# Kernel tuning notes

Hardware: AMD Instinct MI355X
Metric: run time of the kernel (lower is better)

The kernel has to match this reference:

```python
import jax, jax.numpy as jnp
import numpy as np

B, L, D_IN, D_MODEL, D_STATE, D_DISCR, KER = 2, 1024, 512, 1024, 16, 64, 4


def setup_inputs() -> dict:
    ks = jax.random.split(jax.random.key(0), 9)
    s = 0.02
    return {
        "seq": jax.random.normal(ks[0], (B, L, D_IN), jnp.float32),
        "W_in": jax.random.normal(ks[1], (2 * D_MODEL, D_IN), jnp.float32) * s,
        "W_out": jax.random.normal(ks[2], (D_IN, D_MODEL), jnp.float32) * s,
        "W_B": jax.random.normal(ks[3], (D_STATE, D_MODEL), jnp.float32) * s,
        "W_C": jax.random.normal(ks[4], (D_STATE, D_MODEL), jnp.float32) * s,
        "W_D1": jax.random.normal(ks[5], (D_DISCR, D_MODEL), jnp.float32) * s,
        "W_D2": jax.random.normal(ks[6], (D_MODEL, D_DISCR), jnp.float32) * s,
        "conv_w": jax.random.normal(ks[7], (D_MODEL, 1, KER), jnp.float32) * 0.1,
        "conv_b": jax.random.normal(ks[8], (D_MODEL,), jnp.float32) * 0.01,
        "A": jnp.tile(jnp.arange(1, D_STATE + 1, dtype=jnp.float32), (D_MODEL, 1)),
        "D": jnp.ones((D_MODEL,), jnp.float32),
    }


def _causal_depthwise_conv(x, w, b):
    # x: [B, L, D] -> torch Conv1d(groups=D, padding=KER-1) truncated to first L outputs
    x = jnp.swapaxes(x, 1, 2)  # [B, D, L]
    y = jax.lax.conv_general_dilated(
        x, w, window_strides=(1,), padding=[(KER - 1, 0)],
        dimension_numbers=("NCH", "OIH", "NCH"), feature_group_count=D_MODEL)
    y = y + b[None, :, None]
    return jnp.swapaxes(y, 1, 2)  # [B, L, D]


def _ssm(x, W_B, W_C, W_D1, W_D2, A, D):
    # x: [B, L, D]
    exp_negA = jnp.exp(-A)                                  # [D, S]
    Bm = jnp.einsum("bld,sd->bls", x, W_B)                  # [B, L, S]
    Cm = jnp.einsum("bld,sd->bls", x, W_C)                  # [B, L, S]
    delta = jax.nn.softplus(D + jnp.einsum("ble,de->bld", jnp.einsum("bld,ed->ble", x, W_D1), W_D2))  # [B, L, D]
    A_bar = exp_negA[None, None] * delta[..., None]         # [B, L, D, S]
    X = Bm[:, :, None, :] * delta[..., None] * x[..., None]  # [B, L, D, S]

    def comb(c1, c2):
        a1, x1 = c1
        a2, x2 = c2
        return a1 * a2, a2 * x1 + x2

    _, h = jax.lax.associative_scan(comb, (A_bar, X), axis=1)  # h: [B, L, D, S]
    y = jnp.einsum("blds,bls->bld", h, Cm)
    return y + D * x


def reference(seq, W_in, W_out, W_B, W_C, W_D1, W_D2, conv_w, conv_b, A, D):
    ab = jnp.einsum("bli,oi->blo", seq, W_in)   # [B, L, 2*D_MODEL]
    a, b = ab[..., :D_MODEL], ab[..., D_MODEL:]
    a = jax.nn.silu(_causal_depthwise_conv(a, conv_w, conv_b))
    a = _ssm(a, W_B, W_C, W_D1, W_D2, A, D)
    out = a * jax.nn.silu(b)
    return jnp.einsum("bld,od->blo", out, W_out)  # [B, L, D_IN]
```

## Files before the change

### kernel.cpp

```cpp
#include <hip/hip_runtime.h>
#include <hip/hip_bf16.h>

typedef short short8 __attribute__((ext_vector_type(8)));
typedef short short4v __attribute__((ext_vector_type(4)));
typedef float float4v __attribute__((ext_vector_type(4)));

#define B_   2
#define L_   1024
#define DIN  512
#define DM   1024
#define DS   16
#define DD   64
#define KER_ 4
#define NROW (B_*L_)

#define SD   4
#define SC   128
#define SLC  8
#define NSEG 8

__device__ __forceinline__ float silu_f(float v){ return v / (1.f + expf(-v)); }

__device__ __forceinline__ short2 f2bf2(float a, float b) {
  __hip_bfloat162 h = __float22bfloat162_rn(float2{a, b});
  union { __hip_bfloat162 h; short2 s; } u; u.h = h; return u.s;
}
__device__ __forceinline__ short f2bf1(float a) {
  __hip_bfloat16 h = __float2bfloat16(a);
  union { __hip_bfloat16 h; short s; } u; u.h = h; return u.s;
}
__device__ __forceinline__ short8 pack8(const float4& x0, const float4& x1) {
  short2 s0 = f2bf2(x0.x, x0.y), s1 = f2bf2(x0.z, x0.w);
  short2 s2 = f2bf2(x1.x, x1.y), s3 = f2bf2(x1.z, x1.w);
  return short8{ s0.x, s0.y, s1.x, s1.y, s2.x, s2.y, s3.x, s3.y };
}
__device__ __forceinline__ float bf2f(short s) {
  union { unsigned u; float f; } v; v.u = ((unsigned)(unsigned short)s) << 16; return v.f;
}

__global__ __launch_bounds__(512)
void gemm1_k(const float* __restrict__ seq, const float* __restrict__ Win,
             __hip_bfloat16* __restrict__ ab, float* __restrict__ pall) {
  __shared__ short As[128 * 40];
  __shared__ short Bs[128 * 40];
  const int tid  = threadIdx.x;
  {
    int zi = (blockIdx.y * 16 + blockIdx.x) * 1024 + tid * 2;
    if (zi < NROW * 96) { pall[zi] = 0.f; pall[zi + 1] = 0.f; }
  }
  const int lane = tid & 63;
  const int wave = tid >> 6;
  const int r16  = lane & 15;
  const int quad = lane >> 4;
  const int m0 = blockIdx.y * 128;
  const int n0 = blockIdx.x * 128;
  const int wm = wave & 1;
  const int wn = wave >> 1;
  float4v acc[4][2];
#pragma unroll
  for (int i = 0; i < 4; i++)
#pragma unroll
    for (int j = 0; j < 2; j++) acc[i][j] = (float4v){0.f, 0.f, 0.f, 0.f};
  const int row = tid >> 2, q = tid & 3;
  float4 pfA0, pfA1, pfB0, pfB1;
  auto ldu = [&](int k0) {
    const float4* pa = (const float4*)(seq + (size_t)(m0 + row) * DIN + k0 + q * 8);
    pfA0 = pa[0]; pfA1 = pa[1];
    const float4* pb = (const float4*)(Win + (size_t)(n0 + row) * DIN + k0 + q * 8);
    pfB0 = pb[0]; pfB1 = pb[1];
  };
  auto stu = [&]() {
    *(short8*)&As[row * 40 + q * 8] = pack8(pfA0, pfA1);
    *(short8*)&Bs[row * 40 + q * 8] = pack8(pfB0, pfB1);
  };
  ldu(0);
  for (int k0 = 0; k0 < DIN; k0 += 32) {
    stu();
    __syncthreads();
    if (k0 + 32 < DIN) ldu(k0 + 32);
    short8 afr[4], bfr[2];
#pragma unroll
    for (int mi = 0; mi < 4; mi++)
      afr[mi] = *(const short8*)&As[(wm * 64 + mi * 16 + r16) * 40 + quad * 8];
#pragma unroll
    for (int ni = 0; ni < 2; ni++)
      bfr[ni] = *(const short8*)&Bs[(wn * 32 + ni * 16 + r16) * 40 + quad * 8];
#pragma unroll
    for (int mi = 0; mi < 4; mi++)
#pragma unroll
      for (int ni = 0; ni < 2; ni++)
        acc[mi][ni] = __builtin_amdgcn_mfma_f32_16x16x32_bf16(afr[mi], bfr[ni], acc[mi][ni], 0, 0, 0);
    __syncthreads();
  }
#pragma unroll
  for (int mi = 0; mi < 4; mi++)
#pragma unroll
    for (int ni = 0; ni < 2; ni++) {
      int gn = n0 + wn * 32 + ni * 16 + r16;
#pragma unroll
      for (int r = 0; r < 4; r++) {
        int gm = m0 + wm * 64 + mi * 16 + quad * 4 + r;
        ab[(size_t)gm * (2 * DM) + gn] = __float2bfloat16(acc[mi][ni][r]);
      }
    }
}

__global__ __launch_bounds__(256)
void convproj_k(const __hip_bfloat16* __restrict__ ab, const float* __restrict__ cw,
                const float* __restrict__ cb, const float* __restrict__ WB,
                const float* __restrict__ WC, const float* __restrict__ WD1,
                float* __restrict__ xt, short* __restrict__ gt,
                float* __restrict__ pall) {
  __shared__ char smraw[12800];
  const int blk = blockIdx.x;
  const int tid = threadIdx.x;

  if (blk < 1024) {
    short* tile = (short*)smraw;
    const int n0 = (blk & 31) * 64;
    const int d0 = (blk >> 5) * 64;
    const int l0 = n0 & (L_ - 1);
    for (int u = tid; u < 67 * 8; u += 256) {
      int r = u >> 3, c8 = u & 7;
      int l = l0 - 3 + r;
      short8 v = short8{0, 0, 0, 0, 0, 0, 0, 0};
      if (l >= 0 && r < 67)
        v = *(const short8*)(ab + (size_t)(n0 - l0 + l) * (2 * DM) + d0 + c8 * 8);
      *(short8*)&tile[r * 72 + c8 * 8] = v;
    }
    __syncthreads();
    const int i  = tid & 63;
    const int dl = tid >> 6;
    if (d0 < DM) {
#pragma unroll
      for (int p8 = 0; p8 < 2; p8++) {
        const int dc0 = dl * 16 + p8 * 8;
        short8 t0 = *(const short8*)&tile[(i + 0) * 72 + dc0];
        short8 t1 = *(const short8*)&tile[(i + 1) * 72 + dc0];
        short8 t2 = *(const short8*)&tile[(i + 2) * 72 + dc0];
        short8 t3 = *(const short8*)&tile[(i + 3) * 72 + dc0];
#pragma unroll
        for (int e = 0; e < 8; e++) {
          int d = d0 + dc0 + e;
          float4 w = *(const float4*)(cw + d * 4);
          float a = cb[d];
          a += bf2f(t0[e]) * w.x;
          a += bf2f(t1[e]) * w.y;
          a += bf2f(t2[e]) * w.z;
          a += bf2f(t3[e]) * w.w;
          xt[(size_t)d * NROW + n0 + i] = silu_f(a);
        }
      }
    } else {
#pragma unroll
      for (int p8 = 0; p8 < 2; p8++) {
        const int dc0 = dl * 16 + p8 * 8;
        short8 v = *(const short8*)&tile[(i + 3) * 72 + dc0];
#pragma unroll
        for (int e = 0; e < 8; e++)
          gt[(size_t)(d0 - DM + dc0 + e) * NROW + n0 + i] = v[e];
      }
    }
    return;
  }

  short* As = (short*)smraw;
  short* Bs = As + 64 * 40;
  const int b2   = blk - 1024;
  const int lane = tid & 63;
  const int wave = tid >> 6;
  const int r16  = lane & 15;
  const int quad = lane >> 4;
  const int m0   = (b2 & 31) * 64;
  const int kbeg = (b2 >> 5) * 128;
  float4v acc[6];
#pragma unroll
  for (int i = 0; i < 6; i++) acc[i] = (float4v){0.f, 0.f, 0.f, 0.f};

  short8 ta[KER_];
  float4 pf0[2], pf1[2];
  const int arow = tid >> 2, aq = tid & 3;
  const int an = m0 + arow, al = an & (L_ - 1), abq = an >> 10;

  auto ldu_a = [&](int k0) {
#pragma unroll
    for (int t = 0; t < KER_; t++) {
      int ll = al - (KER_ - 1) + t;
      if (ll >= 0)
        ta[t] = *(const short8*)(ab + (size_t)(abq * L_ + ll) * (2 * DM) + k0 + aq * 8);
      else
        ta[t] = short8{0, 0, 0, 0, 0, 0, 0, 0};
    }
  };
  auto stu_a = [&](int k0) {
    float r8[8];
#pragma unroll
    for (int e = 0; e < 8; e++) {
      int d = k0 + aq * 8 + e;
      float4 w = *(const float4*)(cw + d * 4);
      float a = cb[d];
      a += bf2f(ta[0][e]) * w.x;
      a += bf2f(ta[1][e]) * w.y;
      a += bf2f(ta[2][e]) * w.z;
      a += bf2f(ta[3][e]) * w.w;
      r8[e] = silu_f(a);
    }
    *(short8*)&As[arow * 40 + aq * 8] =
        pack8(float4{r8[0], r8[1], r8[2], r8[3]}, float4{r8[4], r8[5], r8[6], r8[7]});
  };
  auto ldu_b = [&](int j, int k0) {
    int u = tid + j * 256;
    if (u >= 640) return;
    int v = u - 256, row = v >> 2, q = v & 3;
    const float* bp = (row < 16) ? (WB + (size_t)row * DM)
                    : (row < 32) ? (WC + (size_t)(row - 16) * DM)
                                 : (WD1 + (size_t)(row - 32) * DM);
    const float4* p = (const float4*)(bp + k0 + q * 8);
    pf0[j - 1] = p[0]; pf1[j - 1] = p[1];
  };
  auto stu_b = [&](int j) {
    int u = tid + j * 256;
    if (u >= 640) return;
    int v = u - 256, row = v >> 2, q = v & 3;
    *(short8*)&Bs[row * 40 + q * 8] = pack8(pf0[j - 1], pf1[j - 1]);
  };

  ldu_a(kbeg); ldu_b(1, kbeg); ldu_b(2, kbeg);
  for (int k0 = kbeg; k0 < kbeg + 128; k0 += 32) {
    stu_a(k0); stu_b(1); stu_b(2);
    __syncthreads();
    if (k0 + 32 < kbeg + 128) { ldu_a(k0 + 32); ldu_b(1, k0 + 32); ldu_b(2, k0 + 32); }
    short8 afr = *(const short8*)&As[(wave * 16 + r16) * 40 + quad * 8];
#pragma unroll
    for (int ni = 0; ni < 6; ni++) {
      short8 bfr = *(const short8*)&Bs[(ni * 16 + r16) * 40 + quad * 8];
      acc[ni] = __builtin_amdgcn_mfma_f32_16x16x32_bf16(afr, bfr, acc[ni], 0, 0, 0);
    }
    __syncthreads();
  }
#pragma unroll
  for (int ni = 0; ni < 6; ni++) {
    int gn = ni * 16 + r16;
#pragma unroll
    for (int r = 0; r < 4; r++) {
      int gm = m0 + wave * 16 + quad * 4 + r;
      atomicAdd(&pall[(size_t)gm * 96 + gn], acc[ni][r]);
    }
  }
}

__global__ __launch_bounds__(256)
void delta_k(const float* __restrict__ t1, const float* __restrict__ WD2,
             const float* __restrict__ Dv, float* __restrict__ dltT) {
  __shared__ short As[64 * 40];
  __shared__ short Bs[64 * 40];
  const int tid  = threadIdx.x;
  const int lane = tid & 63;
  const int wave = tid >> 6;
  const int r16  = lane & 15;
  const int quad = lane >> 4;
  const int m0 = blockIdx.y * 64;
  const int n0 = blockIdx.x * 64;
  const int wm = wave & 1, wn = wave >> 1;
  float4v acc[2][2];
#pragma unroll
  for (int i = 0; i < 2; i++)
#pragma unroll
    for (int j = 0; j < 2; j++) acc[i][j] = (float4v){0.f, 0.f, 0.f, 0.f};
  float4 pf0[2], pf1[2];
  auto ldu = [&](int j, int k0) {
    int u = tid + j * 256;
    const float4* p;
    if (u < 256) { int row = u >> 2, q = u & 3;
      p = (const float4*)(t1 + (size_t)(m0 + row) * 96 + k0 + q * 8);
    } else { int v = u - 256; int row = v >> 2, q = v & 3;
      p = (const float4*)(WD2 + (size_t)(n0 + row) * DD + k0 + q * 8);
    }
    pf0[j] = p[0]; pf1[j] = p[1];
  };
  auto stu = [&](int j) {
    int u = tid + j * 256;
    short8 s = pack8(pf0[j], pf1[j]);
    if (u < 256) { int row = u >> 2, q = u & 3; *(short8*)&As[row * 40 + q * 8] = s; }
    else { int v = u - 256; int row = v >> 2, q = v & 3; *(short8*)&Bs[row * 40 + q * 8] = s; }
  };
  ldu(0, 0); ldu(1, 0);
  for (int k0 = 0; k0 < DD; k0 += 32) {
    stu(0); stu(1);
    __syncthreads();
    if (k0 + 32 < DD) { ldu(0, k0 + 32); ldu(1, k0 + 32); }
    short8 afr[2], bfr[2];
#pragma unroll
    for (int mi = 0; mi < 2; mi++)
      afr[mi] = *(const short8*)&As[(wm * 32 + mi * 16 + r16) * 40 + quad * 8];
#pragma unroll
    for (int ni = 0; ni < 2; ni++)
      bfr[ni] = *(const short8*)&Bs[(wn * 32 + ni * 16 + r16) * 40 + quad * 8];
#pragma unroll
    for (int mi = 0; mi < 2; mi++)
#pragma unroll
      for (int ni = 0; ni < 2; ni++)
        acc[mi][ni] = __builtin_amdgcn_mfma_f32_16x16x32_bf16(afr[mi], bfr[ni], acc[mi][ni], 0, 0, 0);
    __syncthreads();
  }
#pragma unroll
  for (int mi = 0; mi < 2; mi++)
#pragma unroll
    for (int ni = 0; ni < 2; ni++) {
      int gn = n0 + wn * 32 + ni * 16 + r16;
      float dvn = Dv[gn];
#pragma unroll
      for (int r = 0; r < 4; r++) {
        int gm = m0 + wm * 32 + mi * 16 + quad * 4 + r;
        float v = acc[mi][ni][r] + dvn;
        v = fmaxf(v, 0.f) + log1pf(expf(-fabsf(v)));
        dltT[(size_t)gn * NROW + gm] = v;
      }
    }
}

__global__ __launch_bounds__(512, 2)
void scan_fused_k(const float* __restrict__ xt, const float* __restrict__ dltT,
                  const float* __restrict__ pall, const float* __restrict__ A,
                  const float* __restrict__ Dv, const short* __restrict__ gt,
                  short* __restrict__ soutb) {
  __shared__ float Pl[DS * SD][SC + 1];
  __shared__ float Hl[DS * SD][SC + 1];
  __shared__ float Ps[DS * SD][NSEG + 1];
  __shared__ float Hs[DS * SD][NSEG + 1];
  const int blk = blockIdx.x;
  const int b   = blk >> 8;
  const int d0  = (blk & 255) * SD;
  const int dd  = threadIdx.x & (SD - 1);
  const int c   = threadIdx.x >> 2;
  const int d   = d0 + dd;

  float e[DS];
#pragma unroll
  for (int s = 0; s < DS; s++) e[s] = expf(-A[d * DS + s]);

  const int nbase = b * L_ + c * SLC;
  const float* xrow = xt   + (size_t)d * NROW;
  const float* drow = dltT + (size_t)d * NROW;
  const short* grow = gt   + (size_t)d * NROW;

  float h[DS];
#pragma unroll
  for (int s = 0; s < DS; s++) h[s] = 0.f;
  float pdl = 1.f;
#pragma unroll
  for (int q = 0; q < SLC / 4; q++) {
    const int n = nbase + q * 4;
    float4 x4 = *(const float4*)(xrow + n);
    float4 d4 = *(const float4*)(drow + n);
    float4 bq[4][4];
#pragma unroll
    for (int t = 0; t < 4; t++) {
      const float4* pp = (const float4*)(pall + (size_t)(n + t) * 96);
      bq[t][0] = pp[0]; bq[t][1] = pp[1]; bq[t][2] = pp[2]; bq[t][3] = pp[3];
    }
#pragma unroll
    for (int t = 0; t < 4; t++) {
      float dl = (&d4.x)[t], xv = (&x4.x)[t];
      float dx = dl * xv;
      pdl *= dl;
      float bmv[DS] = { bq[t][0].x, bq[t][0].y, bq[t][0].z, bq[t][0].w,
                        bq[t][1].x, bq[t][1].y, bq[t][1].z, bq[t][1].w,
                        bq[t][2].x, bq[t][2].y, bq[t][2].z, bq[t][2].w,
                        bq[t][3].x, bq[t][3].y, bq[t][3].z, bq[t][3].w };
#pragma unroll
      for (int s = 0; s < DS; s++)
        h[s] = (e[s] * dl) * h[s] + bmv[s] * dx;
    }
  }
#pragma unroll
  for (int s = 0; s < DS; s++) {
    float e2 = e[s] * e[s], e4 = e2 * e2, e8 = e4 * e4;
    Pl[dd * DS + s][c] = e8 * pdl;
    Hl[dd * DS + s][c] = h[s];
  }
  __syncthreads();

  {
    const int seg = threadIdx.x >> 6;
    const int cmb = threadIdx.x & 63;
    float* Prow = &Pl[cmb][0];
    float* Hrow = &Hl[cmb][0];
    float Pa = 1.f, Ha = 0.f;
#pragma unroll
    for (int i = 0; i < SC / NSEG; i++) {
      int c2 = seg * (SC / NSEG) + i;
      float p = Prow[c2], hh = Hrow[c2];
      Prow[c2] = Pa;
      Hrow[c2] = Ha;
      Ha = p * Ha + hh;
      Pa *= p;
    }
    Ps[cmb][seg] = Pa;
    Hs[cmb][seg] = Ha;
  }
  __syncthreads();

  if (threadIdx.x < DS * SD) {
    float* Pr = &Ps[threadIdx.x][0];
    float* Hr = &Hs[threadIdx.x][0];
    float H = 0.f;
#pragma unroll
    for (int g = 0; g < NSEG; g++) {
      float p = Pr[g], hh = Hr[g];
      Hr[g] = H;
      H = p * H + hh;
    }
  }
  __syncthreads();

  const float Dd = Dv[d];
  {
    const int g = c >> 4;
#pragma unroll
    for (int s = 0; s < DS; s++)
      h[s] = Pl[dd * DS + s][c] * Hs[dd * DS + s][g] + Hl[dd * DS + s][c];
  }
#pragma unroll
  for (int q = 0; q < SLC / 4; q++) {
    const int n = nbase + q * 4;
    float4 x4 = *(const float4*)(xrow + n);
    float4 d4 = *(const float4*)(drow + n);
    short4v g4 = *(const short4v*)(grow + n);
    float4 bq[4][4], cq[4][4];
#pragma unroll
    for (int t = 0; t < 4; t++) {
      const float4* pp = (const float4*)(pall + (size_t)(n + t) * 96);
      bq[t][0] = pp[0]; bq[t][1] = pp[1]; bq[t][2] = pp[2]; bq[t][3] = pp[3];
      cq[t][0] = pp[4]; cq[t][1] = pp[5]; cq[t][2] = pp[6]; cq[t][3] = pp[7];
    }
#pragma unroll
    for (int t = 0; t < 4; t++) {
      float dl = (&d4.x)[t], xv = (&x4.x)[t];
      float dx = dl * xv;
      float bmv[DS] = { bq[t][0].x, bq[t][0].y, bq[t][0].z, bq[t][0].w,
                        bq[t][1].x, bq[t][1].y, bq[t][1].z, bq[t][1].w,
                        bq[t][2].x, bq[t][2].y, bq[t][2].z, bq[t][2].w,
                        bq[t][3].x, bq[t][3].y, bq[t][3].z, bq[t][3].w };
      float cmv[DS] = { cq[t][0].x, cq[t][0].y, cq[t][0].z, cq[t][0].w,
                        cq[t][1].x, cq[t][1].y, cq[t][1].z, cq[t][1].w,
                        cq[t][2].x, cq[t][2].y, cq[t][2].z, cq[t][2].w,
                        cq[t][3].x, cq[t][3].y, cq[t][3].z, cq[t][3].w };
      float y = 0.f;
#pragma unroll
      for (int s = 0; s < DS; s++) {
        h[s] = (e[s] * dl) * h[s] + bmv[s] * dx;
        y += h[s] * cmv[s];
      }
      y += Dd * xv;
      float gg = bf2f(g4[t]);
      soutb[(size_t)(n + t) * DM + d] = f2bf1(y * silu_f(gg));
    }
  }
}

__global__ __launch_bounds__(256)
void gemm2_k(const short* __restrict__ soutb, const float* __restrict__ Wout,
             float* __restrict__ out) {
  __shared__ short As[64 * 40];
  __shared__ short Bs[64 * 40];
  const int tid  = threadIdx.x;
  const int lane = tid & 63;
  const int wave = tid >> 6;
  const int r16  = lane & 15;
  const int quad = lane >> 4;
  const int m0 = blockIdx.y * 64;
  const int n0 = blockIdx.x * 64;
  const int wm = wave & 1, wn = wave >> 1;
  float4v acc[2][2];
#pragma unroll
  for (int i = 0; i < 2; i++)
#pragma unroll
    for (int j = 0; j < 2; j++) acc[i][j] = (float4v){0.f, 0.f, 0.f, 0.f};
  const int row = tid >> 2, q = tid & 3;
  short8 pa;
  float4 pf0, pf1;
  auto ldu = [&](int k0) {
    pa = *(const short8*)(soutb + (size_t)(m0 + row) * DM + k0 + q * 8);
    const float4* p = (const float4*)(Wout + (size_t)(n0 + row) * DM + k0 + q * 8);
    pf0 = p[0]; pf1 = p[1];
  };
  auto stu = [&]() {
    *(short8*)&As[row * 40 + q * 8] = pa;
    *(short8*)&Bs[row * 40 + q * 8] = pack8(pf0, pf1);
  };
  ldu(0);
  for (int k0 = 0; k0 < DM; k0 += 32) {
    stu();
    __syncthreads();
    if (k0 + 32 < DM) ldu(k0 + 32);
    short8 afr[2], bfr[2];
#pragma unroll
    for (int mi = 0; mi < 2; mi++)
      afr[mi] = *(const short8*)&As[(wm * 32 + mi * 16 + r16) * 40 + quad * 8];
#pragma unroll
    for (int ni = 0; ni < 2; ni++)
      bfr[ni] = *(const short8*)&Bs[(wn * 32 + ni * 16 + r16) * 40 + quad * 8];
#pragma unroll
    for (int mi = 0; mi < 2; mi++)
#pragma unroll
      for (int ni = 0; ni < 2; ni++)
        acc[mi][ni] = __builtin_amdgcn_mfma_f32_16x16x32_bf16(afr[mi], bfr[ni], acc[mi][ni], 0, 0, 0);
    __syncthreads();
  }
#pragma unroll
  for (int mi = 0; mi < 2; mi++)
#pragma unroll
    for (int ni = 0; ni < 2; ni++) {
      int gn = n0 + wn * 32 + ni * 16 + r16;
#pragma unroll
      for (int r = 0; r < 4; r++) {
        int gm = m0 + wm * 32 + mi * 16 + quad * 4 + r;
        out[(size_t)gm * DIN + gn] = acc[mi][ni][r];
      }
    }
}

extern "C" void kernel_launch(void* const* d_in, const int* in_sizes, int n_in,
                              void* d_out, int out_size, void* d_ws, size_t ws_size,
                              hipStream_t stream) {
  const float* seq  = (const float*)d_in[0];
  const float* Win  = (const float*)d_in[1];
  const float* Wout = (const float*)d_in[2];
  const float* WB   = (const float*)d_in[3];
  const float* WC   = (const float*)d_in[4];
  const float* WD1  = (const float*)d_in[5];
  const float* WD2  = (const float*)d_in[6];
  const float* cw   = (const float*)d_in[7];
  const float* cb   = (const float*)d_in[8];
  const float* A    = (const float*)d_in[9];
  const float* Dv   = (const float*)d_in[10];
  float* out = (float*)d_out;

  float* ws = (float*)d_ws;
  __hip_bfloat16* ab = (__hip_bfloat16*)ws;
  float* xt   = ws   + 2097152;
  short* gt   = (short*)(xt + 2097152);
  float* dltT = (float*)(gt + 2097152);
  float* pall = dltT + 2097152;
  short* soutb = (short*)(pall + 196608);
  float* t1   = pall + 32;

  gemm1_k<<<dim3(16, 16), 512, 0, stream>>>(seq, Win, ab, pall);
  convproj_k<<<1280, 256, 0, stream>>>(ab, cw, cb, WB, WC, WD1, xt, gt, pall);
  delta_k<<<dim3(16, 32), 256, 0, stream>>>(t1, WD2, Dv, dltT);
  scan_fused_k<<<B_ * (DM / SD), 512, 0, stream>>>(xt, dltT, pall, A, Dv, gt, soutb);
  gemm2_k<<<dim3(8, 32), 256, 0, stream>>>(soutb, Wout, out);
}
```

Measured before the change: 161.1 us.

## Fuse delta projection into convproj kernel and drop split-K atomics

The delta GEMM kernel is folded into the projection part of convproj_k. Each of 32 projection blocks now runs the full K=1024 reduction for its 64 rows instead of using split-K with atomicAdd, so pall no longer needs zeroing in gemm1 and shrinks to a 32-float stride. The D1 projection stays in shared memory as bf16 and is multiplied by WD2 in-block to write softplus delta directly. This removes one launch, the atomics and the t1 round trip through global memory. The cost is that only 32 blocks do a long serial K loop plus a 1024-column delta loop, which may put them on the critical path.

```diff
diff --git a/kernel.cpp b/kernel.cpp
--- a/kernel.cpp
+++ b/kernel.cpp
@@ -13,6 +13,7 @@
 #define DD   64
 #define KER_ 4
 #define NROW (B_*L_)
+#define PSTR 32
 
 #define SD   4
 #define SC   128
@@ -40,14 +41,10 @@
 
 __global__ __launch_bounds__(512)
 void gemm1_k(const float* __restrict__ seq, const float* __restrict__ Win,
-             __hip_bfloat16* __restrict__ ab, float* __restrict__ pall) {
+             __hip_bfloat16* __restrict__ ab) {
   __shared__ short As[128 * 40];
   __shared__ short Bs[128 * 40];
   const int tid  = threadIdx.x;
-  {
-    int zi = (blockIdx.y * 16 + blockIdx.x) * 1024 + tid * 2;
-    if (zi < NROW * 96) { pall[zi] = 0.f; pall[zi + 1] = 0.f; }
-  }
   const int lane = tid & 63;
   const int wave = tid >> 6;
   const int r16  = lane & 15;
@@ -109,16 +106,18 @@
 void convproj_k(const __hip_bfloat16* __restrict__ ab, const float* __restrict__ cw,
                 const float* __restrict__ cb, const float* __restrict__ WB,
                 const float* __restrict__ WC, const float* __restrict__ WD1,
+                const float* __restrict__ WD2, const float* __restrict__ Dv,
                 float* __restrict__ xt, short* __restrict__ gt,
-                float* __restrict__ pall) {
-  __shared__ char smraw[12800];
+                float* __restrict__ pall, float* __restrict__ dltT) {
+  __shared__ char smraw[18432];
   const int blk = blockIdx.x;
   const int tid = threadIdx.x;
 
-  if (blk < 1024) {
+  if (blk >= 32) {
+    const int cblk = blk - 32;
     short* tile = (short*)smraw;
-    const int n0 = (blk & 31) * 64;
-    const int d0 = (blk >> 5) * 64;
+    const int n0 = (cblk & 31) * 64;
+    const int d0 = (cblk >> 5) * 64;
     const int l0 = n0 & (L_ - 1);
     for (int u = tid; u < 67 * 8; u += 256) {
       int r = u >> 3, c8 = u & 7;
@@ -166,13 +165,11 @@
 
   short* As = (short*)smraw;
   short* Bs = As + 64 * 40;
-  const int b2   = blk - 1024;
   const int lane = tid & 63;
   const int wave = tid >> 6;
   const int r16  = lane & 15;
   const int quad = lane >> 4;
-  const int m0   = (b2 & 31) * 64;
-  const int kbeg = (b2 >> 5) * 128;
+  const int m0   = blk * 64;
   float4v acc[6];
 #pragma unroll
   for (int i = 0; i < 6; i++) acc[i] = (float4v){0.f, 0.f, 0.f, 0.f};
@@ -225,11 +222,11 @@
     *(short8*)&Bs[row * 40 + q * 8] = pack8(pf0[j - 1], pf1[j - 1]);
   };
 
-  ldu_a(kbeg); ldu_b(1, kbeg); ldu_b(2, kbeg);
-  for (int k0 = kbeg; k0 < kbeg + 128; k0 += 32) {
+  ldu_a(0); ldu_b(1, 0); ldu_b(2, 0);
+  for (int k0 = 0; k0 < DM; k0 += 32) {
     stu_a(k0); stu_b(1); stu_b(2);
     __syncthreads();
-    if (k0 + 32 < kbeg + 128) { ldu_a(k0 + 32); ldu_b(1, k0 + 32); ldu_b(2, k0 + 32); }
+    if (k0 + 32 < DM) { ldu_a(k0 + 32); ldu_b(1, k0 + 32); ldu_b(2, k0 + 32); }
     short8 afr = *(const short8*)&As[(wave * 16 + r16) * 40 + quad * 8];
 #pragma unroll
     for (int ni = 0; ni < 6; ni++) {
@@ -238,85 +235,76 @@
     }
     __syncthreads();
   }
-#pragma unroll
-  for (int ni = 0; ni < 6; ni++) {
+
+  short* t1s  = (short*)smraw;
+  short* wd2s = t1s + 64 * 72;
+#pragma unroll
+  for (int ni = 0; ni < 2; ni++) {
     int gn = ni * 16 + r16;
 #pragma unroll
     for (int r = 0; r < 4; r++) {
       int gm = m0 + wave * 16 + quad * 4 + r;
-      atomicAdd(&pall[(size_t)gm * 96 + gn], acc[ni][r]);
-    }
-  }
-}
-
-__global__ __launch_bounds__(256)
-void delta_k(const float* __restrict__ t1, const float* __restrict__ WD2,
-             const float* __restrict__ Dv, float* __restrict__ dltT) {
-  __shared__ short As[64 * 40];
-  __shared__ short Bs[64 * 40];
-  const int tid  = threadIdx.x;
-  const int lane = tid & 63;
-  const int wave = tid >> 6;
-  const int r16  = lane & 15;
-  const int quad = lane >> 4;
-  const int m0 = blockIdx.y * 64;
-  const int n0 = blockIdx.x * 64;
-  const int wm = wave & 1, wn = wave >> 1;
-  float4v acc[2][2];
-#pragma unroll
-  for (int i = 0; i < 2; i++)
-#pragma unroll
-    for (int j = 0; j < 2; j++) acc[i][j] = (float4v){0.f, 0.f, 0.f, 0.f};
-  float4 pf0[2], pf1[2];
-  auto ldu = [&](int j, int k0) {
-    int u = tid + j * 256;
-    const float4* p;
-    if (u < 256) { int row = u >> 2, q = u & 3;
-      p = (const float4*)(t1 + (size_t)(m0 + row) * 96 + k0 + q * 8);
-    } else { int v = u - 256; int row = v >> 2, q = v & 3;
-      p = (const float4*)(WD2 + (size_t)(n0 + row) * DD + k0 + q * 8);
-    }
-    pf0[j] = p[0]; pf1[j] = p[1];
-  };
-  auto stu = [&](int j) {
-    int u = tid + j * 256;
-    short8 s = pack8(pf0[j], pf1[j]);
-    if (u < 256) { int row = u >> 2, q = u & 3; *(short8*)&As[row * 40 + q * 8] = s; }
-    else { int v = u - 256; int row = v >> 2, q = v & 3; *(short8*)&Bs[row * 40 + q * 8] = s; }
-  };
-  ldu(0, 0); ldu(1, 0);
-  for (int k0 = 0; k0 < DD; k0 += 32) {
-    stu(0); stu(1);
-    __syncthreads();
-    if (k0 + 32 < DD) { ldu(0, k0 + 32); ldu(1, k0 + 32); }
-    short8 afr[2], bfr[2];
-#pragma unroll
-    for (int mi = 0; mi < 2; mi++)
-      afr[mi] = *(const short8*)&As[(wm * 32 + mi * 16 + r16) * 40 + quad * 8];
-#pragma unroll
-    for (int ni = 0; ni < 2; ni++)
-      bfr[ni] = *(const short8*)&Bs[(wn * 32 + ni * 16 + r16) * 40 + quad * 8];
-#pragma unroll
-    for (int mi = 0; mi < 2; mi++)
+      pall[(size_t)gm * PSTR + gn] = acc[ni][r];
+    }
+  }
+#pragma unroll
+  for (int ni = 2; ni < 6; ni++) {
+    int col = (ni - 2) * 16 + r16;
+#pragma unroll
+    for (int r = 0; r < 4; r++) {
+      int rowm = wave * 16 + quad * 4 + r;
+      t1s[rowm * 72 + col] = f2bf1(acc[ni][r]);
+    }
+  }
+  __syncthreads();
+
+  const int wm2 = wave & 1, wn2 = wave >> 1;
+  const int w_row = tid >> 2, w_q = tid & 3;
+  for (int dc = 0; dc < DM; dc += 64) {
+    {
+      const float4* p = (const float4*)(WD2 + (size_t)(dc + w_row) * DD + w_q * 16);
+      float4 p0 = p[0], p1 = p[1], p2 = p[2], p3 = p[3];
+      *(short8*)&wd2s[w_row * 72 + w_q * 16]     = pack8(p0, p1);
+      *(short8*)&wd2s[w_row * 72 + w_q * 16 + 8] = pack8(p2, p3);
+    }
+    __syncthreads();
+    float4v a2[2][2];
+#pragma unroll
+    for (int i = 0; i < 2; i++)
+#pragma unroll
+      for (int j = 0; j < 2; j++) a2[i][j] = (float4v){0.f, 0.f, 0.f, 0.f};
+#pragma unroll
+    for (int ks = 0; ks < 64; ks += 32) {
+      short8 afr[2], bfr[2];
+#pragma unroll
+      for (int mi = 0; mi < 2; mi++)
+        afr[mi] = *(const short8*)&t1s[(wm2 * 32 + mi * 16 + r16) * 72 + ks + quad * 8];
 #pragma unroll
       for (int ni = 0; ni < 2; ni++)
-        acc[mi][ni] = __builtin_amdgcn_mfma_f32_16x16x32_bf16(afr[mi], bfr[ni], acc[mi][ni], 0, 0, 0);
-    __syncthreads();
-  }
-#pragma unroll
-  for (int mi = 0; mi < 2; mi++)
+        bfr[ni] = *(const short8*)&wd2s[(wn2 * 32 + ni * 16 + r16) * 72 + ks + quad * 8];
+#pragma unroll
+      for (int mi = 0; mi < 2; mi++)
+#pragma unroll
+        for (int ni = 0; ni < 2; ni++)
+          a2[mi][ni] = __builtin_amdgcn_mfma_f32_16x16x32_bf16(afr[mi], bfr[ni], a2[mi][ni], 0, 0, 0);
+    }
 #pragma unroll
     for (int ni = 0; ni < 2; ni++) {
-      int gn = n0 + wn * 32 + ni * 16 + r16;
-      float dvn = Dv[gn];
-#pragma unroll
-      for (int r = 0; r < 4; r++) {
-        int gm = m0 + wm * 32 + mi * 16 + quad * 4 + r;
-        float v = acc[mi][ni][r] + dvn;
-        v = fmaxf(v, 0.f) + log1pf(expf(-fabsf(v)));
-        dltT[(size_t)gn * NROW + gm] = v;
+      int gd = dc + wn2 * 32 + ni * 16 + r16;
+      float dvn = Dv[gd];
+#pragma unroll
+      for (int mi = 0; mi < 2; mi++) {
+#pragma unroll
+        for (int r = 0; r < 4; r++) {
+          int gm = m0 + wm2 * 32 + mi * 16 + quad * 4 + r;
+          float v = a2[mi][ni][r] + dvn;
+          v = fmaxf(v, 0.f) + log1pf(expf(-fabsf(v)));
+          dltT[(size_t)gd * NROW + gm] = v;
+        }
       }
     }
+    __syncthreads();
+  }
 }
 
 __global__ __launch_bounds__(512, 2)
@@ -356,7 +344,7 @@
     float4 bq[4][4];
 #pragma unroll
     for (int t = 0; t < 4; t++) {
-      const float4* pp = (const float4*)(pall + (size_t)(n + t) * 96);
+      const float4* pp = (const float4*)(pall + (size_t)(n + t) * PSTR);
       bq[t][0] = pp[0]; bq[t][1] = pp[1]; bq[t][2] = pp[2]; bq[t][3] = pp[3];
     }
 #pragma unroll
@@ -430,7 +418,7 @@
     float4 bq[4][4], cq[4][4];
 #pragma unroll
     for (int t = 0; t < 4; t++) {
-      const float4* pp = (const float4*)(pall + (size_t)(n + t) * 96);
+      const float4* pp = (const float4*)(pall + (size_t)(n + t) * PSTR);
       bq[t][0] = pp[0]; bq[t][1] = pp[1]; bq[t][2] = pp[2]; bq[t][3] = pp[3];
       cq[t][0] = pp[4]; cq[t][1] = pp[5]; cq[t][2] = pp[6]; cq[t][3] = pp[7];
     }
@@ -543,12 +531,11 @@
   short* gt   = (short*)(xt + 2097152);
   float* dltT = (float*)(gt + 2097152);
   float* pall = dltT + 2097152;
-  short* soutb = (short*)(pall + 196608);
-  float* t1   = pall + 32;
-
-  gemm1_k<<<dim3(16, 16), 512, 0, stream>>>(seq, Win, ab, pall);
-  convproj_k<<<1280, 256, 0, stream>>>(ab, cw, cb, WB, WC, WD1, xt, gt, pall);
-  delta_k<<<dim3(16, 32), 256, 0, stream>>>(t1, WD2, Dv, dltT);
+  short* soutb = (short*)(pall + NROW * PSTR);
+
+  gemm1_k<<<dim3(16, 16), 512, 0, stream>>>(seq, Win, ab);
+  convproj_k<<<1056, 256, 0, stream>>>(ab, cw, cb, WB, WC, WD1, WD2, Dv,
+                                       xt, gt, pall, dltT);
   scan_fused_k<<<B_ * (DM / SD), 512, 0, stream>>>(xt, dltT, pall, A, Dv, gt, soutb);
   gemm2_k<<<dim3(8, 32), 256, 0, stream>>>(soutb, Wout, out);
 }
```

Measured after the change: 262.0 us. +62.7%, slower.
